# Kernel tuning notes

Hardware: AMD Instinct MI355X
Metric: run time of the kernel (lower is better)

Reference implementation:

```python
import jax, jax.numpy as jnp
import numpy as np

N, E, B = 100000, 640000, 2000
NODE_TYPES, EDGE_TYPES = 16, 5
ND, ED, EMB, L = 256, 128, 256, 3  # node_dim, edge_dim, emb_dim, num encoder blocks


def setup_inputs() -> dict:
    key = jax.random.key(0)
    ks = jax.random.split(key, 20)
    s = 0.02
    inp = {
        "h_node": jax.random.normal(ks[0], (N, NODE_TYPES), jnp.float32),
        "pos_node": jax.random.normal(ks[1], (N, 3), jnp.float32),
        "h_edge": jax.random.normal(ks[2], (E, EDGE_TYPES), jnp.float32),
        "W_node": jax.random.normal(ks[3], (NODE_TYPES, ND), jnp.float32) * s,
        "W_edge": jax.random.normal(ks[4], (EDGE_TYPES, ED), jnp.float32) * s,
        # per-block encoder params (stacked over L blocks)
        "W_eu": jax.random.normal(ks[5], (L, ED + 2 * ND + 1, ED), jnp.float32) * s,
        "b_eu": jnp.zeros((L, ED), jnp.float32),
        "W_msg": jax.random.normal(ks[6], (L, ND + ED, ND), jnp.float32) * s,
        "b_msg": jnp.zeros((L, ND), jnp.float32),
        "W_nu": jax.random.normal(ks[7], (L, 2 * ND, ND), jnp.float32) * s,
        "b_nu": jnp.zeros((L, ND), jnp.float32),
        # final MLP: in=ND+ED, hidden=2*EMB, out=EMB (num_layer=2)
        "Wf1": jax.random.normal(ks[8], (ND + ED, 2 * EMB), jnp.float32) * s,
        "bf1": jnp.zeros((2 * EMB,), jnp.float32),
        "Wf2": jax.random.normal(ks[9], (2 * EMB, EMB), jnp.float32) * s,
        "bf2": jnp.zeros((EMB,), jnp.float32),
        "edge_index": jax.random.randint(ks[10], (2, E), 0, N, jnp.int64),
        "batch_node": jnp.sort(jax.random.randint(ks[11], (N,), 0, B, jnp.int64)),
        "batch_edge": jnp.sort(jax.random.randint(ks[12], (E,), 0, B, jnp.int64)),
    }
    return inp


def _segment_mean(x, ids, num_segments):
    tot = jax.ops.segment_sum(x, ids, num_segments=num_segments)
    cnt = jax.ops.segment_sum(jnp.ones((x.shape[0], 1), x.dtype), ids,
                              num_segments=num_segments)
    return tot / jnp.maximum(cnt, 1.0)


def reference(h_node, pos_node, h_edge, W_node, W_edge, W_eu, b_eu,
              W_msg, b_msg, W_nu, b_nu, Wf1, bf1, Wf2, bf2,
              edge_index, batch_node, batch_edge):
    src, dst = edge_index[0], edge_index[1]
    # embed node / edge type features
    hn = h_node @ W_node            # [N, ND]
    he = h_edge @ W_edge            # [E, ED]
    # NodeEdgeNet: L message-passing blocks with geometric edge feature
    dist = jnp.linalg.norm(pos_node[dst] - pos_node[src], axis=-1,
                           keepdims=True)  # [E, 1]
    for l in range(L):
        e_in = jnp.concatenate([he, hn[src], hn[dst], dist], axis=-1)
        he = jax.nn.relu(e_in @ W_eu[l] + b_eu[l])                 # edge update
        msg = jax.nn.relu(jnp.concatenate([hn[src], he], axis=-1)
                          @ W_msg[l] + b_msg[l])                    # [E, ND]
        agg = jax.ops.segment_sum(msg, dst, num_segments=N)         # [N, ND]
        hn = hn + jax.nn.relu(jnp.concatenate([hn, agg], axis=-1)
                              @ W_nu[l] + b_nu[l])                  # node update
    # per-graph mean pooling (replaces python loop over k with segment mean)
    mean_n = _segment_mean(hn, batch_node, B)   # [B, ND]
    mean_e = _segment_mean(he, batch_edge, B)   # [B, ED]
    h_sub = jnp.concatenate([mean_n, mean_e], axis=-1)  # [B, ND+ED]
    emb = jax.nn.relu(h_sub @ Wf1 + bf1) @ Wf2 + bf2     # [B, EMB]
    return emb, batch_node
```

## Files before the change

### kernel.cpp

```cpp
#include <hip/hip_runtime.h>
#include <hip/hip_bf16.h>
#include <math.h>

#define NN 100000
#define NE 640000
#define NB 2000

typedef __attribute__((ext_vector_type(4))) float v4f;
typedef long long ll64;
#define MFMA8(a, b, c) __builtin_amdgcn_mfma_f32_16x16x32_fp8_fp8(a, b, c, 0, 0, 0)

#define INV_S 0.000244140625f
#define ASCL 16.0f
#define AINV 0.0625f

#if __has_builtin(__builtin_amdgcn_cvt_pk_fp8_f32) && __has_builtin(__builtin_amdgcn_cvt_f32_fp8)
#define HW_FP8 1
#else
#define HW_FP8 0
#endif

__device__ __forceinline__ int IDX(const void* p, size_t i, int is64) {
    return is64 ? (int)((const long long*)p)[i] : ((const int*)p)[i];
}
__device__ __forceinline__ int clampi(int v, int n) {
    return ((unsigned)v < (unsigned)n) ? v : 0;
}

__global__ void k_detect(const int* bn32, int* flag) {
    if (threadIdx.x == 0 && blockIdx.x == 0) {
        int is64 = 1;
        for (int k = 50001; k < 50401; k += 2)
            if (bn32[k] != 0) { is64 = 0; break; }
        *flag = is64;
    }
}

__device__ __forceinline__ unsigned sw_enc_fp8(float x) {
    unsigned s = (__float_as_uint(x) >> 24) & 0x80u;
    float ax = fminf(fabsf(x), 448.f);
    if (ax < 0.015625f) {
        unsigned m = (unsigned)(ax * 512.f + 0.5f);
        return s | m;
    }
    unsigned b = __float_as_uint(ax) + 0x00080000u;
    unsigned e = (b >> 23) - 120u;
    unsigned m = (b >> 20) & 7u;
    unsigned v = (e << 3) | m;
    if (v > 0x7Eu) v = 0x7Eu;
    return s | v;
}
__device__ __forceinline__ float sw_dec_fp8(unsigned b) {
    unsigned s = (b & 0x80u) << 24;
    unsigned e = (b >> 3) & 15u;
    unsigned m = b & 7u;
    if (e) return __uint_as_float(s | ((e + 120u) << 23) | (m << 20));
    float f = (float)m * 0.001953125f;
    return (b & 0x80u) ? -f : f;
}
__device__ __forceinline__ unsigned enc1(float x) {
#if HW_FP8
    return (unsigned)__builtin_amdgcn_cvt_pk_fp8_f32(x, x, 0, false) & 255u;
#else
    return sw_enc_fp8(x);
#endif
}
__device__ __forceinline__ unsigned encpk(float a, float b) {
#if HW_FP8
    return (unsigned)__builtin_amdgcn_cvt_pk_fp8_f32(a, b, 0, false) & 0xFFFFu;
#else
    return sw_enc_fp8(a) | (sw_enc_fp8(b) << 8);
#endif
}
__device__ __forceinline__ float dec1(unsigned b) {
#if HW_FP8
    return __builtin_amdgcn_cvt_f32_fp8((int)b, 0);
#else
    return sw_dec_fp8(b);
#endif
}
__device__ __forceinline__ float bf_f(unsigned short u) {
    return __uint_as_float((unsigned)u << 16);
}
__device__ __forceinline__ unsigned short f_to_bf(float x) {
    __hip_bfloat16 h = __float2bfloat16(x);
    return *(unsigned short*)&h;
}

__global__ __launch_bounds__(256) void k_node_embed(const float* __restrict__ h_node,
                                                    const float* __restrict__ W,
                                                    unsigned char* __restrict__ hn8) {
    __shared__ float sh[8][16];
    int t = threadIdx.x;
    int r0 = blockIdx.x * 8;
    if (t < 128) sh[t >> 4][t & 15] = h_node[r0 * 16 + t];
    float w[16];
#pragma unroll
    for (int k = 0; k < 16; ++k) w[k] = W[k * 256 + t];
    __syncthreads();
#pragma unroll
    for (int r = 0; r < 8; ++r) {
        float acc = 0.f;
#pragma unroll
        for (int k = 0; k < 16; ++k) acc += sh[r][k] * w[k];
        hn8[(size_t)(r0 + r) * 256 + t] = (unsigned char)enc1(ASCL * acc);
    }
}

__global__ __launch_bounds__(256) void k_edge_embed(const float* __restrict__ h_edge,
                                                    const float* __restrict__ W,
                                                    unsigned char* __restrict__ he8) {
    __shared__ float sh[16][5];
    int t = threadIdx.x;
    int e0 = blockIdx.x * 16;
    if (t < 80) sh[t / 5][t % 5] = h_edge[e0 * 5 + t];
    int c = t & 127;
    int es = t >> 7;
    float w[5];
#pragma unroll
    for (int k = 0; k < 5; ++k) w[k] = W[k * 128 + c];
    __syncthreads();
#pragma unroll
    for (int e = 0; e < 8; ++e) {
        int ee = es * 8 + e;
        float acc = 0.f;
#pragma unroll
        for (int k = 0; k < 5; ++k) acc += sh[ee][k] * w[k];
        he8[(size_t)(e0 + ee) * 128 + c] = (unsigned char)enc1(ASCL * acc);
    }
}

__global__ __launch_bounds__(256) void k_dist(const float* __restrict__ pos,
                                              const void* __restrict__ ei,
                                              const int* __restrict__ flag,
                                              float* __restrict__ dist) {
    int e = blockIdx.x * 256 + threadIdx.x;
    if (e >= NE) return;
    int is64 = *flag;
    int s = clampi(IDX(ei, e, is64), NN);
    int d = clampi(IDX(ei, (size_t)NE + e, is64), NN);
    float dx = pos[d * 3 + 0] - pos[s * 3 + 0];
    float dy = pos[d * 3 + 1] - pos[s * 3 + 1];
    float dz = pos[d * 3 + 2] - pos[s * 3 + 2];
    dist[e] = sqrtf(dx * dx + dy * dy + dz * dz);
}

__global__ __launch_bounds__(256) void k_tr_w1(const float* __restrict__ W,
                                               unsigned char* __restrict__ WT) {
    int i = blockIdx.x * 256 + threadIdx.x;
    if (i >= 3 * 128 * 128) return;
    int l = i / 16384, r = i % 16384;
    int n = r / 128, k = r % 128;
    WT[i] = (unsigned char)enc1(256.f * W[(size_t)l * 641 * 128 + (size_t)k * 128 + n]);
}
__global__ __launch_bounds__(256) void k_tr_w2(const float* __restrict__ W,
                                               unsigned char* __restrict__ WT) {
    int i = blockIdx.x * 256 + threadIdx.x;
    if (i >= 3 * 256 * 128) return;
    int l = i / 32768, r = i % 32768;
    int n = r / 128, k = r % 128;
    WT[i] = (unsigned char)enc1(256.f * W[(size_t)l * 384 * 256 + (size_t)(256 + k) * 256 + n]);
}
__global__ __launch_bounds__(256) void k_tr_nu(const float* __restrict__ W,
                                               unsigned char* __restrict__ WT) {
    int i = blockIdx.x * 256 + threadIdx.x;
    if (i >= 3 * 256 * 512) return;
    int l = i / 131072, r = i % 131072;
    int n = r / 512, k = r % 512;
    WT[i] = (unsigned char)enc1(256.f * W[(size_t)l * 512 * 256 + (size_t)k * 256 + n]);
}
__global__ __launch_bounds__(256) void k_tr_pre(const float* __restrict__ Weu,
                                                const float* __restrict__ Wmsg,
                                                unsigned char* __restrict__ WT) {
    int i = blockIdx.x * 256 + threadIdx.x;
    if (i >= 3 * 512 * 256) return;
    int l = i / 131072, r = i % 131072;
    int n = r / 256, k = r % 256;
    float w;
    if (n < 128)      w = Weu[(size_t)l * 641 * 128 + (size_t)(128 + k) * 128 + n];
    else if (n < 256) w = Weu[(size_t)l * 641 * 128 + (size_t)(384 + k) * 128 + (n - 128)];
    else              w = Wmsg[(size_t)l * 384 * 256 + (size_t)k * 256 + (n - 256)];
    WT[i] = (unsigned char)enc1(256.f * w);
}

#define NP_AS 264
__global__ __launch_bounds__(256, 3) void k_node_pre(
    const unsigned char* __restrict__ hn8, const unsigned char* __restrict__ WpreT,
    unsigned char* __restrict__ R) {
    __shared__ unsigned char s_A[64 * NP_AS];
    int t = threadIdx.x;
    int rb = blockIdx.x * 64;
    {
        int row = t >> 2, sb = t & 3;
        int gr = rb + row; if (gr >= NN) gr = NN - 1;
        const uint4* sp = (const uint4*)(hn8 + (size_t)gr * 256 + sb * 64);
        uint4 a = sp[0], b = sp[1], c = sp[2], d = sp[3];
        uint4* dp = (uint4*)&s_A[row * NP_AS + sb * 64];
        dp[0] = a; dp[1] = b; dp[2] = c; dp[3] = d;
    }
    __syncthreads();
    int lane = t & 63, wv = t >> 6, quad = lane >> 4, l16 = lane & 15;
    v4f zero4 = {0.f, 0.f, 0.f, 0.f};
#pragma unroll
    for (int pass = 0; pass < 2; ++pass) {
        int nt0 = wv * 8 + pass * 4;
        v4f acc[4][4];
#pragma unroll
        for (int mt = 0; mt < 4; ++mt)
#pragma unroll
            for (int nl = 0; nl < 4; ++nl) acc[mt][nl] = zero4;
#pragma unroll 2
        for (int k = 0; k < 256; k += 32) {
            int ko = k + quad * 8;
            ll64 b[4];
#pragma unroll
            for (int nl = 0; nl < 4; ++nl)
                b[nl] = *(const ll64*)(WpreT + (size_t)((nt0 + nl) * 16 + l16) * 256 + ko);
#pragma unroll
            for (int mt = 0; mt < 4; ++mt) {
                ll64 a = *(const ll64*)&s_A[(mt * 16 + l16) * NP_AS + ko];
#pragma unroll
                for (int nl = 0; nl < 4; ++nl) acc[mt][nl] = MFMA8(a, b[nl], acc[mt][nl]);
            }
        }
#pragma unroll
        for (int nl = 0; nl < 4; ++nl) {
            int c = (nt0 + nl) * 16 + l16;
#pragma unroll
            for (int mt = 0; mt < 4; ++mt)
#pragma unroll
                for (int rr = 0; rr < 2; ++rr) {
                    int rw0 = mt * 16 + quad * 4 + rr * 2;
                    unsigned pk = encpk(acc[mt][nl][rr * 2] * 0.00390625f,
                                        acc[mt][nl][rr * 2 + 1] * 0.00390625f);
                    if (rb + rw0 < NN)
                        R[(size_t)(rb + rw0) * 512 + c] = (unsigned char)(pk & 255u);
                    if (rb + rw0 + 1 < NN)
                        R[(size_t)(rb + rw0 + 1) * 512 + c] = (unsigned char)(pk >> 8);
                }
        }
    }
}

#define EF_S 136
#define EF_QS 264
#define EF_MS 264
__global__ __launch_bounds__(256, 4) void k_edge_fused(
    unsigned char* __restrict__ he8, const unsigned char* __restrict__ R,
    const float* __restrict__ dist,
    const void* __restrict__ ei, const int* __restrict__ flag,
    const unsigned char* __restrict__ W1T, const float* __restrict__ W_eu,
    const float* __restrict__ b_eu,
    const unsigned char* __restrict__ W2T, const float* __restrict__ b_msg,
    unsigned short* __restrict__ agg) {
    __shared__ __align__(16) unsigned char s_A[32 * EF_S];
    __shared__ __align__(16) unsigned char s_Pd[32 * EF_S];
    __shared__ __align__(16) unsigned char s_Ph[32 * EF_S];
    __shared__ __align__(16) unsigned char s_Q[32 * EF_QS];
    __shared__ __align__(16) unsigned short s_msg[32 * EF_MS];
    __shared__ float s_dist[32];
    __shared__ int s_dsti[32];
    int t = threadIdx.x;
    int eb = blockIdx.x * 32;
    int is64 = *flag;
    int row = t >> 3, sb = t & 7;
    int sid = clampi(IDX(ei, (size_t)(eb + row), is64), NN);
    int did = clampi(IDX(ei, (size_t)NE + eb + row, is64), NN);
    if (t < 32) {
        s_dsti[t] = clampi(IDX(ei, (size_t)NE + eb + t, is64), NN);
        s_dist[t] = dist[eb + t];
    }
    *(uint4*)&s_A[row * EF_S + sb * 16] =
        *(const uint4*)(he8 + (size_t)(eb + row) * 128 + sb * 16);
    *(uint4*)&s_Ph[row * EF_S + sb * 16] =
        *(const uint4*)(R + (size_t)sid * 512 + sb * 16);
    *(uint4*)&s_Pd[row * EF_S + sb * 16] =
        *(const uint4*)(R + (size_t)did * 512 + 128 + sb * 16);
    {
        const uint4* qp = (const uint4*)(R + (size_t)sid * 512 + 256 + sb * 32);
        uint4 q0 = qp[0], q1 = qp[1];
        *(uint4*)&s_Q[row * EF_QS + sb * 32] = q0;
        *(uint4*)&s_Q[row * EF_QS + sb * 32 + 16] = q1;
    }
    int lane = t & 63, wv = t >> 6, quad = lane >> 4, l16 = lane & 15;
    int n0 = wv * 2;
    const unsigned char* B0 = W1T + (size_t)(n0 * 16 + l16) * 128 + quad * 8;
    ll64 Brg[4][2];
#pragma unroll
    for (int kk = 0; kk < 4; ++kk) {
        Brg[kk][0] = *(const ll64*)(B0 + kk * 32);
        Brg[kk][1] = *(const ll64*)(B0 + 2048 + kk * 32);
    }
    __syncthreads();

    v4f zero4 = {0.f, 0.f, 0.f, 0.f};
    v4f acc[2][2];
    acc[0][0] = zero4; acc[0][1] = zero4; acc[1][0] = zero4; acc[1][1] = zero4;
#pragma unroll
    for (int kk = 0; kk < 4; ++kk) {
        int ko = kk * 32 + quad * 8;
#pragma unroll
        for (int mt = 0; mt < 2; ++mt) {
            ll64 a = *(const ll64*)&s_A[(mt * 16 + l16) * EF_S + ko];
            acc[mt][0] = MFMA8(a, Brg[kk][0], acc[mt][0]);
            acc[mt][1] = MFMA8(a, Brg[kk][1], acc[mt][1]);
        }
    }
#pragma unroll
    for (int nl = 0; nl < 2; ++nl) {
        int c = (n0 + nl) * 16 + l16;
        float w640 = W_eu[640 * 128 + c];
        float bb = b_eu[c];
#pragma unroll
        for (int mt = 0; mt < 2; ++mt)
#pragma unroll
            for (int rr = 0; rr < 2; ++rr) {
                int rw0 = mt * 16 + quad * 4 + rr * 2;
                int rw1 = rw0 + 1;
                float S0 = (dec1(s_Ph[rw0 * EF_S + c]) +
                            dec1(s_Pd[rw0 * EF_S + c])) * AINV;
                float S1 = (dec1(s_Ph[rw1 * EF_S + c]) +
                            dec1(s_Pd[rw1 * EF_S + c])) * AINV;
                float v0 = fmaxf(acc[mt][nl][rr * 2] * INV_S + S0 +
                                 s_dist[rw0] * w640 + bb, 0.f);
                float v1 = fmaxf(acc[mt][nl][rr * 2 + 1] * INV_S + S1 +
                                 s_dist[rw1] * w640 + bb, 0.f);
                unsigned pk = encpk(ASCL * v0, ASCL * v1);
                unsigned char q0 = (unsigned char)(pk & 255u);
                unsigned char q1 = (unsigned char)(pk >> 8);
                s_Ph[rw0 * EF_S + c] = q0;
                s_Ph[rw1 * EF_S + c] = q1;
                he8[(size_t)(eb + rw0) * 128 + c] = q0;
                he8[(size_t)(eb + rw1) * 128 + c] = q1;
            }
    }
    __syncthreads();

    v4f mac[2][4];
#pragma unroll
    for (int nl = 0; nl < 4; ++nl) { mac[0][nl] = zero4; mac[1][nl] = zero4; }
    int q0n = wv * 4;
#pragma unroll
    for (int kk = 0; kk < 4; ++kk) {
        int ko = kk * 32 + quad * 8;
        ll64 b[4];
#pragma unroll
        for (int nl = 0; nl < 4; ++nl)
            b[nl] = *(const ll64*)(W2T + (size_t)((q0n + nl) * 16 + l16) * 128 + ko);
#pragma unroll
        for (int mt = 0; mt < 2; ++mt) {
            ll64 a = *(const ll64*)&s_Ph[(mt * 16 + l16) * EF_S + ko];
#pragma unroll
            for (int nl = 0; nl < 4; ++nl) mac[mt][nl] = MFMA8(a, b[nl], mac[mt][nl]);
        }
    }
#pragma unroll
    for (int nl = 0; nl < 4; ++nl) {
        int c = (q0n + nl) * 16 + l16;
        float bm = b_msg[c];
#pragma unroll
        for (int mt = 0; mt < 2; ++mt)
#pragma unroll
            for (int r = 0; r < 4; ++r) {
                int rw = mt * 16 + quad * 4 + r;
                float qv = dec1(s_Q[rw * EF_QS + c]) * AINV;
                float v = fmaxf(mac[mt][nl][r] * INV_S + qv + bm, 0.f);
                s_msg[rw * EF_MS + c] = f_to_bf(v);
            }
    }
    __syncthreads();
#pragma unroll
    for (int i = 0; i < 16; ++i) {
        int p = i * 256 + t;
        int rw = p >> 7;
        int cp = p & 127;
        unsigned v = *(const unsigned*)&s_msg[rw * EF_MS + cp * 2];
        if (v) {
            __hip_bfloat162 pv = *(__hip_bfloat162*)&v;
            unsafeAtomicAdd((__hip_bfloat162*)&agg[(size_t)s_dsti[rw] * 256 + cp * 2], pv);
        }
    }
}

#define NL_AS 520
__global__ __launch_bounds__(256, 3) void k_node_layer(
    unsigned char* __restrict__ hn8, const unsigned short* __restrict__ agg,
    const unsigned char* __restrict__ WnuT, const float* __restrict__ b) {
    __shared__ unsigned char s_A[64 * NL_AS];
    int t = threadIdx.x;
    int rb = blockIdx.x * 64;
    {
        int row = t >> 2, sb = t & 3;
        int gr = rb + row; if (gr >= NN) gr = NN - 1;
        const uint4* sp = (const uint4*)(hn8 + (size_t)gr * 256 + sb * 64);
        uint4 a = sp[0], b2 = sp[1], c = sp[2], d = sp[3];
        uint4* dp = (uint4*)&s_A[row * NL_AS + sb * 64];
        dp[0] = a; dp[1] = b2; dp[2] = c; dp[3] = d;
        const unsigned short* ap = agg + (size_t)gr * 256 + sb * 64;
        unsigned char* dq = &s_A[row * NL_AS + 256 + sb * 64];
#pragma unroll
        for (int j = 0; j < 64; j += 2) {
            unsigned pk = encpk(ASCL * bf_f(ap[j]), ASCL * bf_f(ap[j + 1]));
            *(unsigned short*)&dq[j] = (unsigned short)pk;
        }
    }
    __syncthreads();
    int lane = t & 63, wv = t >> 6, quad = lane >> 4, l16 = lane & 15;
    v4f zero4 = {0.f, 0.f, 0.f, 0.f};
    v4f acc[4][4];
#pragma unroll
    for (int mt = 0; mt < 4; ++mt)
#pragma unroll
        for (int nl = 0; nl < 4; ++nl) acc[mt][nl] = zero4;
    int q0 = wv * 4;
#pragma unroll 2
    for (int k = 0; k < 512; k += 32) {
        int ko = k + quad * 8;
        ll64 b2[4];
#pragma unroll
        for (int nl = 0; nl < 4; ++nl)
            b2[nl] = *(const ll64*)(WnuT + (size_t)((q0 + nl) * 16 + l16) * 512 + ko);
#pragma unroll
        for (int mt = 0; mt < 4; ++mt) {
            ll64 a = *(const ll64*)&s_A[(mt * 16 + l16) * NL_AS + ko];
#pragma unroll
            for (int nl = 0; nl < 4; ++nl) acc[mt][nl] = MFMA8(a, b2[nl], acc[mt][nl]);
        }
    }
#pragma unroll
    for (int nl = 0; nl < 4; ++nl) {
        int c = (q0 + nl) * 16 + l16;
        float bv = b[c];
#pragma unroll
        for (int mt = 0; mt < 4; ++mt)
#pragma unroll
            for (int rr = 0; rr < 2; ++rr) {
                int rw0 = mt * 16 + quad * 4 + rr * 2;
                float o0 = dec1(s_A[rw0 * NL_AS + c]) * AINV;
                float o1 = dec1(s_A[(rw0 + 1) * NL_AS + c]) * AINV;
                float v0 = o0 + fmaxf(acc[mt][nl][rr * 2] * INV_S + bv, 0.f);
                float v1 = o1 + fmaxf(acc[mt][nl][rr * 2 + 1] * INV_S + bv, 0.f);
                unsigned pk = encpk(ASCL * v0, ASCL * v1);
                if (rb + rw0 < NN)
                    hn8[(size_t)(rb + rw0) * 256 + c] = (unsigned char)(pk & 255u);
                if (rb + rw0 + 1 < NN)
                    hn8[(size_t)(rb + rw0 + 1) * 256 + c] = (unsigned char)(pk >> 8);
            }
    }
}

__device__ __forceinline__ int lbound(const void* a, int n, int v, int is64) {
    int lo = 0, hi = n;
    while (lo < hi) {
        int mid = (lo + hi) >> 1;
        if (IDX(a, mid, is64) < v) lo = mid + 1; else hi = mid;
    }
    return lo;
}

__global__ __launch_bounds__(512) void k_pool_mlp(
    const unsigned char* __restrict__ hn8, const unsigned char* __restrict__ he8,
    const void* __restrict__ bn, const void* __restrict__ be,
    const int* __restrict__ flag,
    const float* __restrict__ Wf1, const float* __restrict__ bf1,
    const float* __restrict__ Wf2, const float* __restrict__ bf2,
    float* __restrict__ out) {
    __shared__ float s_sub[384];
    __shared__ float s_hid[512];
    int b = blockIdx.x;
    int t = threadIdx.x;
    int is64 = *flag;
    if (t < 256) {
        int lo = lbound(bn, NN, b, is64), hi = lbound(bn, NN, b + 1, is64);
        float s = 0.f;
        for (int i = lo; i < hi; ++i) s += dec1(hn8[(size_t)i * 256 + t]);
        s_sub[t] = s * AINV / fmaxf((float)(hi - lo), 1.f);
    } else if (t < 384) {
        int c = t - 256;
        int lo = lbound(be, NE, b, is64), hi = lbound(be, NE, b + 1, is64);
        float s = 0.f;
        for (int i = lo; i < hi; ++i) s += dec1(he8[(size_t)i * 128 + c]);
        s_sub[256 + c] = s * AINV / fmaxf((float)(hi - lo), 1.f);
    }
    __syncthreads();
    float hacc = bf1[t];
    for (int k = 0; k < 384; ++k) hacc += s_sub[k] * Wf1[k * 512 + t];
    s_hid[t] = fmaxf(hacc, 0.f);
    __syncthreads();
    if (t < 256) {
        float o = bf2[t];
        for (int k = 0; k < 512; ++k) o += s_hid[k] * Wf2[k * 256 + t];
        out[(size_t)b * 256 + t] = o;
    }
}

__global__ __launch_bounds__(256) void k_write_batch(const void* __restrict__ bn,
                                                     const int* __restrict__ flag,
                                                     float* __restrict__ out) {
    int i = blockIdx.x * 256 + threadIdx.x;
    if (i < NN) out[(size_t)NB * 256 + i] = (float)IDX(bn, i, *flag);
}

__global__ __launch_bounds__(256) void k_fill(float* __restrict__ p, int n, float v) {
    int i = blockIdx.x * 256 + threadIdx.x;
    if (i < n) p[i] = v;
}

extern "C" void kernel_launch(void* const* d_in, const int* in_sizes, int n_in,
                              void* d_out, int out_size, void* d_ws, size_t ws_size,
                              hipStream_t stream) {
    const float* h_node = (const float*)d_in[0];
    const float* pos    = (const float*)d_in[1];
    const float* h_edge = (const float*)d_in[2];
    const float* W_node = (const float*)d_in[3];
    const float* W_edge = (const float*)d_in[4];
    const float* W_eu   = (const float*)d_in[5];
    const float* b_eu   = (const float*)d_in[6];
    const float* W_msg  = (const float*)d_in[7];
    const float* b_msg  = (const float*)d_in[8];
    const float* W_nu   = (const float*)d_in[9];
    const float* b_nu   = (const float*)d_in[10];
    const float* Wf1    = (const float*)d_in[11];
    const float* bf1    = (const float*)d_in[12];
    const float* Wf2    = (const float*)d_in[13];
    const float* bf2    = (const float*)d_in[14];
    const void* ei = d_in[15];
    const void* bn = d_in[16];
    const void* be = d_in[17];

    float* out = (float*)d_out;

    const size_t SZ_FLAG = 256;
    const size_t SZ_HN   = (size_t)NN * 256;
    const size_t SZ_HE   = (size_t)NE * 128;
    const size_t SZ_AGG  = (size_t)NN * 256 * 2;
    const size_t SZ_DIST = (size_t)NE * 4;
    const size_t SZ_R    = (size_t)NN * 512;
    const size_t SZ_W1   = (size_t)3 * 128 * 128;
    const size_t SZ_W2   = (size_t)3 * 256 * 128;
    const size_t SZ_WNU  = (size_t)3 * 256 * 512;
    const size_t SZ_WPRE = (size_t)3 * 512 * 256;
    const size_t NEED = SZ_FLAG + SZ_HN + SZ_HE + SZ_AGG + SZ_DIST + SZ_R +
                        SZ_W1 + SZ_W2 + SZ_WNU + SZ_WPRE;

    char* ws = (char*)d_ws;
    int* flag = (int*)ws;                       ws += SZ_FLAG;
    unsigned char* hn8 = (unsigned char*)ws;    ws += SZ_HN;
    unsigned char* he8 = (unsigned char*)ws;    ws += SZ_HE;
    unsigned short* agg = (unsigned short*)ws;  ws += SZ_AGG;
    float* dist = (float*)ws;                   ws += SZ_DIST;
    unsigned char* R = (unsigned char*)ws;      ws += SZ_R;
    unsigned char* W1T = (unsigned char*)ws;    ws += SZ_W1;
    unsigned char* W2T = (unsigned char*)ws;    ws += SZ_W2;
    unsigned char* WnuT = (unsigned char*)ws;   ws += SZ_WNU;
    unsigned char* WpreT = (unsigned char*)ws;  ws += SZ_WPRE;

    if (ws_size < NEED) {
        float enc = -(100000.0f + (float)(ws_size >> 20));
        k_detect<<<1, 64, 0, stream>>>((const int*)bn, flag);
        k_fill<<<(NB * 256 + 255) / 256, 256, 0, stream>>>(out, NB * 256, enc);
        k_write_batch<<<(NN + 255) / 256, 256, 0, stream>>>(bn, flag, out);
        return;
    }

    k_detect<<<1, 64, 0, stream>>>((const int*)bn, flag);
    k_tr_w1<<<(3 * 128 * 128 + 255) / 256, 256, 0, stream>>>(W_eu, W1T);
    k_tr_w2<<<(3 * 256 * 128 + 255) / 256, 256, 0, stream>>>(W_msg, W2T);
    k_tr_nu<<<(3 * 256 * 512 + 255) / 256, 256, 0, stream>>>(W_nu, WnuT);
    k_tr_pre<<<(3 * 512 * 256 + 255) / 256, 256, 0, stream>>>(W_eu, W_msg, WpreT);
    k_node_embed<<<NN / 8, 256, 0, stream>>>(h_node, W_node, hn8);
    k_edge_embed<<<NE / 16, 256, 0, stream>>>(h_edge, W_edge, he8);
    k_dist<<<(NE + 255) / 256, 256, 0, stream>>>(pos, ei, flag, dist);

    for (int l = 0; l < 3; ++l) {
        hipMemsetAsync(agg, 0, SZ_AGG, stream);
        k_node_pre<<<(NN + 63) / 64, 256, 0, stream>>>(
            hn8, WpreT + (size_t)l * 512 * 256, R);
        k_edge_fused<<<NE / 32, 256, 0, stream>>>(
            he8, R, dist, ei, flag,
            W1T + (size_t)l * 128 * 128, W_eu + (size_t)l * 641 * 128,
            b_eu + (size_t)l * 128,
            W2T + (size_t)l * 256 * 128, b_msg + (size_t)l * 256, agg);
        k_node_layer<<<(NN + 63) / 64, 256, 0, stream>>>(
            hn8, agg, WnuT + (size_t)l * 256 * 512, b_nu + (size_t)l * 256);
    }

    k_pool_mlp<<<NB, 512, 0, stream>>>(hn8, he8, bn, be, flag,
                                       Wf1, bf1, Wf2, bf2, out);
    k_write_batch<<<(NN + 255) / 256, 256, 0, stream>>>(bn, flag, out);
}
```

Measured before the change: 1.779 ms.

## Sort edges by destination and pre-reduce messages before atomic scatter

Builds a destination-sorted edge permutation (histogram, single-block scan, atomic placement) and stores edge features, src/dst indices and distances in sorted order. The edge kernel then sums consecutive same-destination rows in registers before issuing bf16 atomics, which cuts atomic traffic and contention on agg. Edge pooling is redirected through the inverse permutation. The added preprocessing kernels and the serial single-block scan cost extra time, and sorting by destination scatters source-row gathers and makes pooling reads of he8 random.

```diff
diff --git a/kernel.cpp b/kernel.cpp
--- a/kernel.cpp
+++ b/kernel.cpp
@@ -109,11 +109,16 @@
 
 __global__ __launch_bounds__(256) void k_edge_embed(const float* __restrict__ h_edge,
                                                     const float* __restrict__ W,
+                                                    const int* __restrict__ perm,
                                                     unsigned char* __restrict__ he8) {
     __shared__ float sh[16][5];
     int t = threadIdx.x;
     int e0 = blockIdx.x * 16;
-    if (t < 80) sh[t / 5][t % 5] = h_edge[e0 * 5 + t];
+    if (t < 80) {
+        int row = t / 5, col = t % 5;
+        int e = perm[e0 + row];
+        sh[row][col] = h_edge[(size_t)e * 5 + col];
+    }
     int c = t & 127;
     int es = t >> 7;
     float w[5];
@@ -128,21 +133,6 @@
         for (int k = 0; k < 5; ++k) acc += sh[ee][k] * w[k];
         he8[(size_t)(e0 + ee) * 128 + c] = (unsigned char)enc1(ASCL * acc);
     }
-}
-
-__global__ __launch_bounds__(256) void k_dist(const float* __restrict__ pos,
-                                              const void* __restrict__ ei,
-                                              const int* __restrict__ flag,
-                                              float* __restrict__ dist) {
-    int e = blockIdx.x * 256 + threadIdx.x;
-    if (e >= NE) return;
-    int is64 = *flag;
-    int s = clampi(IDX(ei, e, is64), NN);
-    int d = clampi(IDX(ei, (size_t)NE + e, is64), NN);
-    float dx = pos[d * 3 + 0] - pos[s * 3 + 0];
-    float dy = pos[d * 3 + 1] - pos[s * 3 + 1];
-    float dz = pos[d * 3 + 2] - pos[s * 3 + 2];
-    dist[e] = sqrtf(dx * dx + dy * dy + dz * dz);
 }
 
 __global__ __launch_bounds__(256) void k_tr_w1(const float* __restrict__ W,
@@ -181,6 +171,62 @@
     else if (n < 256) w = Weu[(size_t)l * 641 * 128 + (size_t)(384 + k) * 128 + (n - 128)];
     else              w = Wmsg[(size_t)l * 384 * 256 + (size_t)k * 256 + (n - 256)];
     WT[i] = (unsigned char)enc1(256.f * w);
+}
+
+__global__ __launch_bounds__(256) void k_hist(const void* __restrict__ ei,
+                                              const int* __restrict__ flag,
+                                              int* __restrict__ hist) {
+    int e = blockIdx.x * 256 + threadIdx.x;
+    if (e >= NE) return;
+    int d = clampi(IDX(ei, (size_t)NE + e, *flag), NN);
+    atomicAdd(&hist[d], 1);
+}
+__global__ __launch_bounds__(1024) void k_scan(const int* __restrict__ hist,
+                                               int* __restrict__ rowptr) {
+    __shared__ int part[1024];
+    int t = threadIdx.x;
+    const int C = 98;
+    int s = 0;
+    for (int j = 0; j < C; ++j) {
+        int i = t * C + j;
+        if (i < NN) s += hist[i];
+    }
+    part[t] = s;
+    __syncthreads();
+    if (t == 0) {
+        int run = 0;
+        for (int i = 0; i < 1024; ++i) { int v = part[i]; part[i] = run; run += v; }
+    }
+    __syncthreads();
+    int run = part[t];
+    for (int j = 0; j < C; ++j) {
+        int i = t * C + j;
+        if (i < NN) { rowptr[i] = run; run += hist[i]; }
+    }
+}
+__global__ __launch_bounds__(256) void k_perm(const void* __restrict__ ei,
+                                              const int* __restrict__ flag,
+                                              const float* __restrict__ pos,
+                                              int* __restrict__ cursor,
+                                              int* __restrict__ perm,
+                                              int* __restrict__ inv,
+                                              int* __restrict__ srcs,
+                                              int* __restrict__ dsts,
+                                              float* __restrict__ dist_s) {
+    int e = blockIdx.x * 256 + threadIdx.x;
+    if (e >= NE) return;
+    int is64 = *flag;
+    int s = clampi(IDX(ei, (size_t)e, is64), NN);
+    int d = clampi(IDX(ei, (size_t)NE + e, is64), NN);
+    int p = atomicAdd(&cursor[d], 1);
+    perm[p] = e;
+    inv[e] = p;
+    srcs[p] = s;
+    dsts[p] = d;
+    float dx = pos[d * 3 + 0] - pos[s * 3 + 0];
+    float dy = pos[d * 3 + 1] - pos[s * 3 + 1];
+    float dz = pos[d * 3 + 2] - pos[s * 3 + 2];
+    dist_s[p] = sqrtf(dx * dx + dy * dy + dz * dz);
 }
 
 #define NP_AS 264
@@ -247,8 +293,8 @@
 #define EF_MS 264
 __global__ __launch_bounds__(256, 4) void k_edge_fused(
     unsigned char* __restrict__ he8, const unsigned char* __restrict__ R,
-    const float* __restrict__ dist,
-    const void* __restrict__ ei, const int* __restrict__ flag,
+    const float* __restrict__ dist_s,
+    const int* __restrict__ srcs, const int* __restrict__ dsts,
     const unsigned char* __restrict__ W1T, const float* __restrict__ W_eu,
     const float* __restrict__ b_eu,
     const unsigned char* __restrict__ W2T, const float* __restrict__ b_msg,
@@ -262,13 +308,12 @@
     __shared__ int s_dsti[32];
     int t = threadIdx.x;
     int eb = blockIdx.x * 32;
-    int is64 = *flag;
     int row = t >> 3, sb = t & 7;
-    int sid = clampi(IDX(ei, (size_t)(eb + row), is64), NN);
-    int did = clampi(IDX(ei, (size_t)NE + eb + row, is64), NN);
+    int sid = srcs[eb + row];
+    int did = dsts[eb + row];
     if (t < 32) {
-        s_dsti[t] = clampi(IDX(ei, (size_t)NE + eb + t, is64), NN);
-        s_dist[t] = dist[eb + t];
+        s_dsti[t] = dsts[eb + t];
+        s_dist[t] = dist_s[eb + t];
     }
     *(uint4*)&s_A[row * EF_S + sb * 16] =
         *(const uint4*)(he8 + (size_t)(eb + row) * 128 + sb * 16);
@@ -369,15 +414,32 @@
             }
     }
     __syncthreads();
-#pragma unroll
-    for (int i = 0; i < 16; ++i) {
-        int p = i * 256 + t;
-        int rw = p >> 7;
-        int cp = p & 127;
-        unsigned v = *(const unsigned*)&s_msg[rw * EF_MS + cp * 2];
-        if (v) {
-            __hip_bfloat162 pv = *(__hip_bfloat162*)&v;
-            unsafeAtomicAdd((__hip_bfloat162*)&agg[(size_t)s_dsti[rw] * 256 + cp * 2], pv);
+    {
+        int cp = t & 127;
+        int half = t >> 7;
+        int r0 = half * 16, r1 = r0 + 16;
+        float ax = 0.f, ay = 0.f;
+        int cur = s_dsti[r0];
+        for (int rw = r0; rw < r1; ++rw) {
+            int d2 = s_dsti[rw];
+            if (d2 != cur) {
+                if (ax != 0.f || ay != 0.f) {
+                    __hip_bfloat162 pv;
+                    pv.x = __float2bfloat16(ax);
+                    pv.y = __float2bfloat16(ay);
+                    unsafeAtomicAdd((__hip_bfloat162*)&agg[(size_t)cur * 256 + cp * 2], pv);
+                }
+                ax = 0.f; ay = 0.f; cur = d2;
+            }
+            unsigned v = *(const unsigned*)&s_msg[rw * EF_MS + cp * 2];
+            ax += bf_f((unsigned short)(v & 0xFFFFu));
+            ay += bf_f((unsigned short)(v >> 16));
+        }
+        if (ax != 0.f || ay != 0.f) {
+            __hip_bfloat162 pv;
+            pv.x = __float2bfloat16(ax);
+            pv.y = __float2bfloat16(ay);
+            unsafeAtomicAdd((__hip_bfloat162*)&agg[(size_t)cur * 256 + cp * 2], pv);
         }
     }
 }
@@ -460,6 +522,7 @@
 
 __global__ __launch_bounds__(512) void k_pool_mlp(
     const unsigned char* __restrict__ hn8, const unsigned char* __restrict__ he8,
+    const int* __restrict__ inv,
     const void* __restrict__ bn, const void* __restrict__ be,
     const int* __restrict__ flag,
     const float* __restrict__ Wf1, const float* __restrict__ bf1,
@@ -479,7 +542,8 @@
         int c = t - 256;
         int lo = lbound(be, NE, b, is64), hi = lbound(be, NE, b + 1, is64);
         float s = 0.f;
-        for (int i = lo; i < hi; ++i) s += dec1(he8[(size_t)i * 128 + c]);
+        for (int i = lo; i < hi; ++i)
+            s += dec1(he8[(size_t)inv[i] * 128 + c]);
         s_sub[256 + c] = s * AINV / fmaxf((float)(hi - lo), 1.f);
     }
     __syncthreads();
@@ -534,13 +598,20 @@
     const size_t SZ_HN   = (size_t)NN * 256;
     const size_t SZ_HE   = (size_t)NE * 128;
     const size_t SZ_AGG  = (size_t)NN * 256 * 2;
-    const size_t SZ_DIST = (size_t)NE * 4;
     const size_t SZ_R    = (size_t)NN * 512;
+    const size_t SZ_PERM = (size_t)NE * 4;
+    const size_t SZ_INV  = (size_t)NE * 4;
+    const size_t SZ_SRC  = (size_t)NE * 4;
+    const size_t SZ_DST  = (size_t)NE * 4;
+    const size_t SZ_DS   = (size_t)NE * 4;
+    const size_t SZ_PTR  = 512 * 1024;
+    const size_t SZ_CUR  = 512 * 1024;
     const size_t SZ_W1   = (size_t)3 * 128 * 128;
     const size_t SZ_W2   = (size_t)3 * 256 * 128;
     const size_t SZ_WNU  = (size_t)3 * 256 * 512;
     const size_t SZ_WPRE = (size_t)3 * 512 * 256;
-    const size_t NEED = SZ_FLAG + SZ_HN + SZ_HE + SZ_AGG + SZ_DIST + SZ_R +
+    const size_t NEED = SZ_FLAG + SZ_HN + SZ_HE + SZ_AGG + SZ_R + SZ_PERM +
+                        SZ_INV + SZ_SRC + SZ_DST + SZ_DS + SZ_PTR + SZ_CUR +
                         SZ_W1 + SZ_W2 + SZ_WNU + SZ_WPRE;
 
     char* ws = (char*)d_ws;
@@ -548,8 +619,14 @@
     unsigned char* hn8 = (unsigned char*)ws;    ws += SZ_HN;
     unsigned char* he8 = (unsigned char*)ws;    ws += SZ_HE;
     unsigned short* agg = (unsigned short*)ws;  ws += SZ_AGG;
-    float* dist = (float*)ws;                   ws += SZ_DIST;
     unsigned char* R = (unsigned char*)ws;      ws += SZ_R;
+    int* perm = (int*)ws;                       ws += SZ_PERM;
+    int* inv = (int*)ws;                        ws += SZ_INV;
+    int* srcs = (int*)ws;                       ws += SZ_SRC;
+    int* dsts = (int*)ws;                       ws += SZ_DST;
+    float* dist_s = (float*)ws;                 ws += SZ_DS;
+    int* rowptr = (int*)ws;                     ws += SZ_PTR;
+    int* cursor = (int*)ws;                     ws += SZ_CUR;
     unsigned char* W1T = (unsigned char*)ws;    ws += SZ_W1;
     unsigned char* W2T = (unsigned char*)ws;    ws += SZ_W2;
     unsigned char* WnuT = (unsigned char*)ws;   ws += SZ_WNU;
@@ -569,15 +646,21 @@
     k_tr_nu<<<(3 * 256 * 512 + 255) / 256, 256, 0, stream>>>(W_nu, WnuT);
     k_tr_pre<<<(3 * 512 * 256 + 255) / 256, 256, 0, stream>>>(W_eu, W_msg, WpreT);
     k_node_embed<<<NN / 8, 256, 0, stream>>>(h_node, W_node, hn8);
-    k_edge_embed<<<NE / 16, 256, 0, stream>>>(h_edge, W_edge, he8);
-    k_dist<<<(NE + 255) / 256, 256, 0, stream>>>(pos, ei, flag, dist);
+
+    hipMemsetAsync(cursor, 0, (size_t)NN * 4, stream);
+    k_hist<<<(NE + 255) / 256, 256, 0, stream>>>(ei, flag, cursor);
+    k_scan<<<1, 1024, 0, stream>>>(cursor, rowptr);
+    hipMemcpyAsync(cursor, rowptr, (size_t)NN * 4, hipMemcpyDeviceToDevice, stream);
+    k_perm<<<(NE + 255) / 256, 256, 0, stream>>>(ei, flag, pos, cursor, perm,
+                                                 inv, srcs, dsts, dist_s);
+    k_edge_embed<<<NE / 16, 256, 0, stream>>>(h_edge, W_edge, perm, he8);
 
     for (int l = 0; l < 3; ++l) {
         hipMemsetAsync(agg, 0, SZ_AGG, stream);
         k_node_pre<<<(NN + 63) / 64, 256, 0, stream>>>(
             hn8, WpreT + (size_t)l * 512 * 256, R);
         k_edge_fused<<<NE / 32, 256, 0, stream>>>(
-            he8, R, dist, ei, flag,
+            he8, R, dist_s, srcs, dsts,
             W1T + (size_t)l * 128 * 128, W_eu + (size_t)l * 641 * 128,
             b_eu + (size_t)l * 128,
             W2T + (size_t)l * 256 * 128, b_msg + (size_t)l * 256, agg);
@@ -585,7 +668,7 @@
             hn8, agg, WnuT + (size_t)l * 256 * 512, b_nu + (size_t)l * 256);
     }
 
-    k_pool_mlp<<<NB, 512, 0, stream>>>(hn8, he8, bn, be, flag,
+    k_pool_mlp<<<NB, 512, 0, stream>>>(hn8, he8, inv, bn, be, flag,
                                        Wf1, bf1, Wf2, bf2, out);
     k_write_batch<<<(NN + 255) / 256, 256, 0, stream>>>(bn, flag, out);
 }
```

Result: slower. 1.931 ms (+8.6%).
